# Kernel tuning notes

Measured on AMD Instinct MI355X. Metric: run time of the kernel, lower is better.

Reference implementation:

```python
import jax, jax.numpy as jnp
import numpy as np

LATENT = 512
MEL = 80


def _lstm(x, Wk, Wr, b):
    # x: [B, T, Din]; Keras gate order i, f, g(cell), o
    B = x.shape[0]
    D = Wr.shape[0]
    h0 = jnp.zeros((B, D), x.dtype)
    c0 = jnp.zeros((B, D), x.dtype)

    def step(carry, xt):
        h, c = carry
        z = xt @ Wk + h @ Wr + b  # [B, 4D]
        i, f, g, o = jnp.split(z, 4, axis=-1)
        i = jax.nn.sigmoid(i)
        f = jax.nn.sigmoid(f)
        g = jnp.tanh(g)
        o = jax.nn.sigmoid(o)
        c = f * c + i * g
        h = o * jnp.tanh(c)
        return (h, c), h

    (h_f, c_f), hs = jax.lax.scan(step, (h0, c0), x.transpose(1, 0, 2))
    return hs.transpose(1, 0, 2), h_f, c_f  # [B,T,D], [B,D], [B,D]


def setup_inputs() -> dict:
    key = jax.random.key(0)
    ks = jax.random.split(key, 10)
    B, Td, Te, Din, D = 8, 256, 256, MEL, LATENT
    s = lambda k, shp, fan: jax.random.normal(k, shp, jnp.float32) / np.sqrt(fan)
    return {
        "inputs": jax.random.normal(ks[0], (B, Td, Din), jnp.float32),
        "attended_inputs": jax.random.normal(ks[1], (B, Te, D), jnp.float32),
        "lstm_Wk": s(ks[2], (Din, 4 * D), Din),
        "lstm_Wr": s(ks[3], (D, 4 * D), D),
        "lstm_b": jnp.zeros((4 * D,), jnp.float32),
        "W1": s(ks[4], (D, D), D),
        "b1": jnp.zeros((D,), jnp.float32),
        "W3": s(ks[5], (D, 1), D),
        "b3": jnp.zeros((1,), jnp.float32),
        "Wout": s(ks[6], (2 * D, MEL), 2 * D),
        "bout": jnp.zeros((MEL,), jnp.float32),
    }


def reference(inputs, attended_inputs, lstm_Wk, lstm_Wr, lstm_b, W1, b1, W3, b3, Wout, bout):
    x, state_h, state_c = _lstm(inputs, lstm_Wk, lstm_Wr, lstm_b)  # [B,Td,D]
    # NOTE: original code uses dense1 for BOTH projections (dense2 unused)
    half1 = (attended_inputs @ W1 + b1)[:, None, :, :]   # [B,1,Te,D]
    half2 = (x @ W1 + b1)[:, :, None, :]                 # [B,Td,1,D]
    scores = jnp.squeeze(jnp.tanh(half1 + half2) @ W3 + b3, -1)  # [B,Td,Te]
    attn = jax.nn.softmax(scores, axis=-1)
    weighted = jnp.einsum('bde,bef->bdf', attn, attended_inputs)  # [B,Td,D]
    x = jnp.concatenate([x, weighted], axis=2)           # [B,Td,2D]
    out = x @ Wout + bout                                 # [B,Td,MEL]
    return out, state_h, state_c
```

## Files before the change

### kernel.cpp

```cpp
#include <hip/hip_runtime.h>
#include <cstdint>
#include <cmath>

#define TD 256
#define TE 256
#define NB 8
#define DD 512
#define DIN 80
#define NMEL 80

typedef unsigned long long u64;

__device__ __forceinline__ void gemm_body(const float* __restrict__ A,
    const float* __restrict__ B, const float* __restrict__ bias,
    float* __restrict__ C, int N, int K, int m0, int n0)
{
    __shared__ float As[64][17];
    __shared__ __align__(16) float Bs[16][64];
    const int tid = threadIdx.x;
    const int tx = tid & 15, ty = tid >> 4;
    float acc[4][4] = {};
    for (int k0 = 0; k0 < K; k0 += 16) {
#pragma unroll
        for (int i = 0; i < 4; ++i) {
            int lin = tid + i * 256;
            int k = lin & 15, m = lin >> 4;
            As[m][k] = A[(size_t)(m0 + m) * K + k0 + k];
        }
#pragma unroll
        for (int i = 0; i < 4; ++i) {
            int lin = tid + i * 256;
            int n = lin & 63, k = lin >> 6;
            Bs[k][n] = B[(size_t)(k0 + k) * N + n0 + n];
        }
        __syncthreads();
#pragma unroll
        for (int kk = 0; kk < 16; ++kk) {
            float a0 = As[ty * 4 + 0][kk], a1 = As[ty * 4 + 1][kk];
            float a2 = As[ty * 4 + 2][kk], a3 = As[ty * 4 + 3][kk];
            const float4 b4 = *(const float4*)&Bs[kk][tx * 4];
            acc[0][0] += a0 * b4.x; acc[0][1] += a0 * b4.y; acc[0][2] += a0 * b4.z; acc[0][3] += a0 * b4.w;
            acc[1][0] += a1 * b4.x; acc[1][1] += a1 * b4.y; acc[1][2] += a1 * b4.z; acc[1][3] += a1 * b4.w;
            acc[2][0] += a2 * b4.x; acc[2][1] += a2 * b4.y; acc[2][2] += a2 * b4.z; acc[2][3] += a2 * b4.w;
            acc[3][0] += a3 * b4.x; acc[3][1] += a3 * b4.y; acc[3][2] += a3 * b4.z; acc[3][3] += a3 * b4.w;
        }
        __syncthreads();
    }
    const float4 bv = *(const float4*)&bias[n0 + tx * 4];
#pragma unroll
    for (int i = 0; i < 4; ++i) {
        float4 o;
        o.x = acc[i][0] + bv.x; o.y = acc[i][1] + bv.y;
        o.z = acc[i][2] + bv.z; o.w = acc[i][3] + bv.w;
        *(float4*)&C[(size_t)(m0 + ty * 4 + i) * N + n0 + tx * 4] = o;
    }
}

__global__ __launch_bounds__(256) void gemm_bias_k(const float* __restrict__ A,
    const float* __restrict__ B, const float* __restrict__ bias,
    float* __restrict__ C, int N, int K)
{
    gemm_body(A, B, bias, C, N, K, blockIdx.y * 64, blockIdx.x * 64);
}

__global__ __launch_bounds__(256) void fused_pre_k(
    const float* __restrict__ inputs, const float* __restrict__ Wk,
    const float* __restrict__ lb, float* __restrict__ Zx,
    const float* __restrict__ att, const float* __restrict__ W1,
    const float* __restrict__ b1, float* __restrict__ half1)
{
    int wg = blockIdx.x;
    if (wg < 1024) {
        gemm_body(inputs, Wk, lb, Zx, 2048, 80, (wg >> 5) * 64, (wg & 31) * 64);
    } else {
        wg -= 1024;
        gemm_body(att, W1, b1, half1, 512, 512, (wg >> 3) * 64, (wg & 7) * 64);
    }
}

__global__ __launch_bounds__(256, 1) void lstm_k(const float* __restrict__ Zx,
    const float* __restrict__ Wr, float* __restrict__ hs,
    u64* __restrict__ hpub,
    float* __restrict__ outh, float* __restrict__ outc)
{
    __shared__ __align__(16) float h_s[512];
    __shared__ float part[256];
    const int b = blockIdx.x & 7;
    const int g = blockIdx.x >> 3;
    const int tid = threadIdx.x;
    const int wv = tid >> 6;
    const int lane = tid & 63;
    const int gcol = ((lane >> 4) << 9) | (g << 4) | (lane & 15);
    const int col = (g << 4) | (lane & 15);

    float w[128];
    {
        const float* wb = Wr + (size_t)(wv * 128) * 2048 + gcol;
#pragma unroll
        for (int i = 0; i < 128; ++i) w[i] = wb[(size_t)i * 2048];
    }
    float creg = 0.f, hlast = 0.f;
    u64* const pub0 = hpub + (size_t)b * 512;
    u64* const pub1 = hpub + (size_t)(8 + b) * 512;

    for (int t = 0; t < TD; ++t) {
        float zx = 0.f;
        if (wv == 0) zx = Zx[(size_t)(b * TD + t) * 2048 + gcol];

        {
            u64* const pr = (t & 1) ? pub1 : pub0;
            const unsigned stag = (unsigned)t;
            u64 v0 = 0, v1 = 0;
            bool d0 = false, d1 = false;
            for (;;) {
                if (!d0) { v0 = __hip_atomic_load(pr + tid, __ATOMIC_RELAXED, __HIP_MEMORY_SCOPE_AGENT);
                           d0 = ((unsigned)(v0 >> 32) == stag); }
                if (!d1) { v1 = __hip_atomic_load(pr + tid + 256, __ATOMIC_RELAXED, __HIP_MEMORY_SCOPE_AGENT);
                           d1 = ((unsigned)(v1 >> 32) == stag); }
                if (d0 && d1) break;
                __builtin_amdgcn_s_sleep(1);
            }
            h_s[tid]       = __uint_as_float((unsigned)v0);
            h_s[tid + 256] = __uint_as_float((unsigned)v1);
        }
        __syncthreads();

        float acc = 0.f;
        {
            const float4* h4 = (const float4*)(h_s + (wv << 7));
#pragma unroll
            for (int i = 0; i < 32; ++i) {
                float4 h = h4[i];
                acc += w[4 * i + 0] * h.x;
                acc += w[4 * i + 1] * h.y;
                acc += w[4 * i + 2] * h.z;
                acc += w[4 * i + 3] * h.w;
            }
        }
        part[tid] = acc;
        __syncthreads();
        if (wv == 0) {
            float z = part[lane] + part[64 + lane] + part[128 + lane] + part[192 + lane] + zx;
            float zf = __shfl(z, lane + 16);
            float zg = __shfl(z, lane + 32);
            float zo = __shfl(z, lane + 48);
            if (lane < 16) {
                float ig = 1.f / (1.f + expf(-z));
                float fg = 1.f / (1.f + expf(-zf));
                float gg = tanhf(zg);
                float og = 1.f / (1.f + expf(-zo));
                creg = fg * creg + ig * gg;
                hlast = og * tanhf(creg);
                u64 pv = ((u64)(unsigned)(t + 1) << 32) | (u64)__float_as_uint(hlast);
                u64* const pw = (t & 1) ? pub0 : pub1;
                __hip_atomic_store(pw + col, pv, __ATOMIC_RELAXED, __HIP_MEMORY_SCOPE_AGENT);
                hs[(size_t)(b * TD + t) * 512 + col] = hlast;
            }
        }
    }
    if (wv == 0 && lane < 16) {
        outh[b * 512 + col] = hlast;
        outc[b * 512 + col] = creg;
    }
}

__global__ __launch_bounds__(256) void attn_k(const float* __restrict__ half1,
    const float* __restrict__ half2, const float* __restrict__ att,
    const float* __restrict__ W3, const float* __restrict__ b3,
    float* __restrict__ wgt)
{
    __shared__ __align__(16) float h2s[4][512];
    __shared__ float h1s[256 * 33];
    __shared__ __align__(16) float sc[4][256];
    __shared__ __align__(16) float av[8][512];
    const int tid = threadIdx.x;
    const int bb = blockIdx.x >> 6;
    const int d0 = (blockIdx.x & 63) * 4;
    const float C2 = 2.885390081777927f;

#pragma unroll
    for (int i = 0; i < 8; ++i) {
        int lin = tid + i * 256;
        int r = lin >> 9, k = lin & 511;
        h2s[r][k] = half2[(size_t)(bb * TD + d0 + r) * 512 + k] * C2;
    }

    float accs[4] = {0.f, 0.f, 0.f, 0.f};
    for (int kc = 0; kc < 512; kc += 32) {
#pragma unroll
        for (int i = 0; i < 32; ++i) {
            int lin = tid + i * 256;
            int e = lin >> 5, kk = lin & 31;
            h1s[e * 33 + kk] = half1[(size_t)(bb * TE + e) * 512 + kc + kk] * C2;
        }
        __syncthreads();
        const float* myh1 = h1s + tid * 33;
#pragma unroll 8
        for (int kk = 0; kk < 32; ++kk) {
            float u = myh1[kk];
            float w = W3[kc + kk];
#pragma unroll
            for (int r = 0; r < 4; ++r) {
                float t = 1.f - 2.f * __builtin_amdgcn_rcpf(__builtin_amdgcn_exp2f(u + h2s[r][kc + kk]) + 1.f);
                accs[r] += t * w;
            }
        }
        __syncthreads();
    }
    {
        const float b3v = b3[0];
#pragma unroll
        for (int r = 0; r < 4; ++r) sc[r][tid] = accs[r] + b3v;
    }
    __syncthreads();
    {
        const int r = tid >> 6, l = tid & 63;
        float4 v = *(const float4*)&sc[r][l * 4];
        float mx = fmaxf(fmaxf(v.x, v.y), fmaxf(v.z, v.w));
#pragma unroll
        for (int off = 32; off; off >>= 1) mx = fmaxf(mx, __shfl_xor(mx, off));
        const float L2E = 1.44269504089f;
        float e0 = __builtin_amdgcn_exp2f((v.x - mx) * L2E);
        float e1 = __builtin_amdgcn_exp2f((v.y - mx) * L2E);
        float e2 = __builtin_amdgcn_exp2f((v.z - mx) * L2E);
        float e3 = __builtin_amdgcn_exp2f((v.w - mx) * L2E);
        float s = e0 + e1 + e2 + e3;
#pragma unroll
        for (int off = 32; off; off >>= 1) s += __shfl_xor(s, off);
        float inv = 1.f / s;
        float4 p; p.x = e0 * inv; p.y = e1 * inv; p.z = e2 * inv; p.w = e3 * inv;
        *(float4*)&sc[r][l * 4] = p;
    }
    __syncthreads();
    float acc[4][2] = {};
    for (int e0 = 0; e0 < TE; e0 += 8) {
#pragma unroll
        for (int i = 0; i < 16; ++i) {
            int lin = tid + i * 256;
            int e = lin >> 9, k = lin & 511;
            av[e][k] = att[(size_t)(bb * TE + e0 + e) * 512 + k];
        }
        __syncthreads();
#pragma unroll
        for (int ee = 0; ee < 8; ++ee) {
            float x0 = av[ee][tid], x1 = av[ee][tid + 256];
#pragma unroll
            for (int r = 0; r < 4; ++r) {
                float p = sc[r][e0 + ee];
                acc[r][0] += p * x0;
                acc[r][1] += p * x1;
            }
        }
        __syncthreads();
    }
#pragma unroll
    for (int r = 0; r < 4; ++r) {
        wgt[(size_t)(bb * TD + d0 + r) * 512 + tid] = acc[r][0];
        wgt[(size_t)(bb * TD + d0 + r) * 512 + tid + 256] = acc[r][1];
    }
}

__global__ __launch_bounds__(256) void outgemm_k(const float* __restrict__ x,
    const float* __restrict__ wgt, const float* __restrict__ Wout,
    const float* __restrict__ bout, float* __restrict__ out)
{
    __shared__ float As[64][17];
    __shared__ float Bs[16][80];
    const int tid = threadIdx.x;
    const int tx = tid & 15, ty = tid >> 4;
    const int m0 = blockIdx.x * 64;
    const int ks = blockIdx.y;
    float acc[4][5] = {};
    for (int kt = 0; kt < 16; ++kt) {
        const int k0 = ks * 256 + kt * 16;
        const float* src = (k0 < 512) ? x : wgt;
        const int kk0 = (k0 < 512) ? k0 : (k0 - 512);
#pragma unroll
        for (int i = 0; i < 4; ++i) {
            int lin = tid + i * 256;
            int k = lin & 15, m = lin >> 4;
            As[m][k] = src[(size_t)(m0 + m) * 512 + kk0 + k];
        }
#pragma unroll
        for (int i = 0; i < 5; ++i) {
            int lin = tid + i * 256;
            int n = lin % 80, k = lin / 80;
            Bs[k][n] = Wout[(size_t)(k0 + k) * 80 + n];
        }
        __syncthreads();
#pragma unroll
        for (int kk = 0; kk < 16; ++kk) {
            float a[4], bv[5];
#pragma unroll
            for (int i = 0; i < 4; ++i) a[i] = As[ty * 4 + i][kk];
#pragma unroll
            for (int j = 0; j < 5; ++j) bv[j] = Bs[kk][tx * 5 + j];
#pragma unroll
            for (int i = 0; i < 4; ++i)
#pragma unroll
                for (int j = 0; j < 5; ++j) acc[i][j] += a[i] * bv[j];
        }
        __syncthreads();
    }
#pragma unroll
    for (int i = 0; i < 4; ++i) {
#pragma unroll
        for (int j = 0; j < 5; ++j) {
            float v = acc[i][j];
            if (ks == 0) v += bout[tx * 5 + j];
            atomicAdd(&out[(size_t)(m0 + ty * 4 + i) * 80 + tx * 5 + j], v);
        }
    }
}

extern "C" void kernel_launch(void* const* d_in, const int* in_sizes, int n_in,
                              void* d_out, int out_size, void* d_ws, size_t ws_size,
                              hipStream_t stream)
{
    (void)in_sizes; (void)n_in; (void)out_size; (void)ws_size;
    const float* inputs = (const float*)d_in[0];
    const float* att    = (const float*)d_in[1];
    const float* Wk     = (const float*)d_in[2];
    const float* Wr     = (const float*)d_in[3];
    const float* lb     = (const float*)d_in[4];
    const float* W1     = (const float*)d_in[5];
    const float* b1     = (const float*)d_in[6];
    const float* W3     = (const float*)d_in[7];
    const float* b3     = (const float*)d_in[8];
    const float* Wout   = (const float*)d_in[9];
    const float* bout   = (const float*)d_in[10];

    float* out  = (float*)d_out;
    float* outh = out + 2048 * 80;
    float* outc = outh + 8 * 512;

    char* ws = (char*)d_ws;
    float* Zx    = (float*)(ws);
    float* half1 = (float*)(ws + (16u << 20));
    float* half2 = (float*)(ws + (20u << 20));
    float* hsx   = (float*)(ws + (24u << 20));
    float* wgt   = (float*)(ws + (28u << 20));
    u64*   hpub  = (u64*)(ws + (32u << 20));

    (void)hipMemsetAsync(ws + (32u << 20), 0, 2 * 8 * 512 * sizeof(u64), stream);
    (void)hipMemsetAsync(d_out, 0, (size_t)2048 * 80 * 4, stream);

    fused_pre_k<<<dim3(1280), 256, 0, stream>>>(inputs, Wk, lb, Zx, att, W1, b1, half1);

    void* args[] = { (void*)&Zx, (void*)&Wr, (void*)&hsx, (void*)&hpub,
                     (void*)&outh, (void*)&outc };
    (void)hipLaunchCooperativeKernel((void*)lstm_k, dim3(256), dim3(256), args, 0, stream);

    gemm_bias_k<<<dim3(8, 32), 256, 0, stream>>>(hsx, W1, b1, half2, 512, 512);
    attn_k<<<dim3(512), 256, 0, stream>>>(half1, half2, att, W3, b3, wgt);
    outgemm_k<<<dim3(32, 4), 256, 0, stream>>>(hsx, wgt, Wout, bout, out);
}
```

Measured before the change: 912.1 us.

## Fuse all stages into one cooperative persistent kernel with grid syncs

Merges the pre-GEMM, LSTM recurrence, half2 GEMM, attention and output GEMM into a single cooperative kernel of 256 workgroups. Stages are separated by grid.sync, and shared memory is carved from one pool. This removes four kernel launches and the gaps between them. In exchange, every stage now runs at 256 workgroups with launch_bounds(256,1) and a large shared pool, which can hurt the GEMM and attention phases that previously used more blocks and higher occupancy. The old multi-kernel path is kept as a fallback if the cooperative launch fails.

```diff
diff --git a/kernel.cpp b/kernel.cpp
--- a/kernel.cpp
+++ b/kernel.cpp
@@ -1,6 +1,9 @@
 #include <hip/hip_runtime.h>
+#include <hip/hip_cooperative_groups.h>
 #include <cstdint>
 #include <cmath>
+
+namespace cg = cooperative_groups;
 
 #define TD 256
 #define TE 256
@@ -11,12 +14,14 @@
 
 typedef unsigned long long u64;
 
+#define SMEM_POOL_BYTES 46080
+
 __device__ __forceinline__ void gemm_body(const float* __restrict__ A,
     const float* __restrict__ B, const float* __restrict__ bias,
-    float* __restrict__ C, int N, int K, int m0, int n0)
-{
-    __shared__ float As[64][17];
-    __shared__ __align__(16) float Bs[16][64];
+    float* __restrict__ C, int N, int K, int m0, int n0, char* sm)
+{
+    float (*As)[17] = (float(*)[17])sm;
+    float (*Bs)[64] = (float(*)[64])(sm + 4352);
     const int tid = threadIdx.x;
     const int tx = tid & 15, ty = tid >> 4;
     float acc[4][4] = {};
@@ -56,37 +61,15 @@
     }
 }
 
-__global__ __launch_bounds__(256) void gemm_bias_k(const float* __restrict__ A,
-    const float* __restrict__ B, const float* __restrict__ bias,
-    float* __restrict__ C, int N, int K)
-{
-    gemm_body(A, B, bias, C, N, K, blockIdx.y * 64, blockIdx.x * 64);
-}
-
-__global__ __launch_bounds__(256) void fused_pre_k(
-    const float* __restrict__ inputs, const float* __restrict__ Wk,
-    const float* __restrict__ lb, float* __restrict__ Zx,
-    const float* __restrict__ att, const float* __restrict__ W1,
-    const float* __restrict__ b1, float* __restrict__ half1)
-{
-    int wg = blockIdx.x;
-    if (wg < 1024) {
-        gemm_body(inputs, Wk, lb, Zx, 2048, 80, (wg >> 5) * 64, (wg & 31) * 64);
-    } else {
-        wg -= 1024;
-        gemm_body(att, W1, b1, half1, 512, 512, (wg >> 3) * 64, (wg & 7) * 64);
-    }
-}
-
-__global__ __launch_bounds__(256, 1) void lstm_k(const float* __restrict__ Zx,
+__device__ __forceinline__ void lstm_body(const float* __restrict__ Zx,
     const float* __restrict__ Wr, float* __restrict__ hs,
-    u64* __restrict__ hpub,
-    float* __restrict__ outh, float* __restrict__ outc)
-{
-    __shared__ __align__(16) float h_s[512];
-    __shared__ float part[256];
-    const int b = blockIdx.x & 7;
-    const int g = blockIdx.x >> 3;
+    u64* __restrict__ hpub, float* __restrict__ outh, float* __restrict__ outc,
+    int wg, char* sm)
+{
+    float* h_s  = (float*)sm;
+    float* part = (float*)(sm + 2048);
+    const int b = wg & 7;
+    const int g = wg >> 3;
     const int tid = threadIdx.x;
     const int wv = tid >> 6;
     const int lane = tid & 63;
@@ -164,18 +147,16 @@
     }
 }
 
-__global__ __launch_bounds__(256) void attn_k(const float* __restrict__ half1,
+__device__ __forceinline__ void attn_body(const float* __restrict__ half1,
     const float* __restrict__ half2, const float* __restrict__ att,
     const float* __restrict__ W3, const float* __restrict__ b3,
-    float* __restrict__ wgt)
-{
-    __shared__ __align__(16) float h2s[4][512];
-    __shared__ float h1s[256 * 33];
-    __shared__ __align__(16) float sc[4][256];
-    __shared__ __align__(16) float av[8][512];
+    float* __restrict__ wgt, int bb, int d0, char* sm)
+{
+    float (*h2s)[512] = (float(*)[512])sm;
+    float (*sc)[256]  = (float(*)[256])(sm + 8192);
+    float *h1s        = (float*)(sm + 12288);
+    float (*av)[512]  = (float(*)[512])(sm + 12288);
     const int tid = threadIdx.x;
-    const int bb = blockIdx.x >> 6;
-    const int d0 = (blockIdx.x & 63) * 4;
     const float C2 = 2.885390081777927f;
 
 #pragma unroll
@@ -260,16 +241,15 @@
     }
 }
 
-__global__ __launch_bounds__(256) void outgemm_k(const float* __restrict__ x,
+__device__ __forceinline__ void outgemm_body(const float* __restrict__ x,
     const float* __restrict__ wgt, const float* __restrict__ Wout,
-    const float* __restrict__ bout, float* __restrict__ out)
-{
-    __shared__ float As[64][17];
-    __shared__ float Bs[16][80];
+    const float* __restrict__ bout, float* __restrict__ out, int m0, int ks,
+    char* sm)
+{
+    float (*As2)[17] = (float(*)[17])sm;
+    float (*Bs2)[80] = (float(*)[80])(sm + 4352);
     const int tid = threadIdx.x;
     const int tx = tid & 15, ty = tid >> 4;
-    const int m0 = blockIdx.x * 64;
-    const int ks = blockIdx.y;
     float acc[4][5] = {};
     for (int kt = 0; kt < 16; ++kt) {
         const int k0 = ks * 256 + kt * 16;
@@ -279,22 +259,22 @@
         for (int i = 0; i < 4; ++i) {
             int lin = tid + i * 256;
             int k = lin & 15, m = lin >> 4;
-            As[m][k] = src[(size_t)(m0 + m) * 512 + kk0 + k];
+            As2[m][k] = src[(size_t)(m0 + m) * 512 + kk0 + k];
         }
 #pragma unroll
         for (int i = 0; i < 5; ++i) {
             int lin = tid + i * 256;
             int n = lin % 80, k = lin / 80;
-            Bs[k][n] = Wout[(size_t)(k0 + k) * 80 + n];
+            Bs2[k][n] = Wout[(size_t)(k0 + k) * 80 + n];
         }
         __syncthreads();
 #pragma unroll
         for (int kk = 0; kk < 16; ++kk) {
             float a[4], bv[5];
 #pragma unroll
-            for (int i = 0; i < 4; ++i) a[i] = As[ty * 4 + i][kk];
-#pragma unroll
-            for (int j = 0; j < 5; ++j) bv[j] = Bs[kk][tx * 5 + j];
+            for (int i = 0; i < 4; ++i) a[i] = As2[ty * 4 + i][kk];
+#pragma unroll
+            for (int j = 0; j < 5; ++j) bv[j] = Bs2[kk][tx * 5 + j];
 #pragma unroll
             for (int i = 0; i < 4; ++i)
 #pragma unroll
@@ -311,6 +291,96 @@
             atomicAdd(&out[(size_t)(m0 + ty * 4 + i) * 80 + tx * 5 + j], v);
         }
     }
+}
+
+__global__ __launch_bounds__(256, 1) void mega_k(
+    const float* __restrict__ inputs, const float* __restrict__ Wk,
+    const float* __restrict__ lb, const float* __restrict__ att,
+    const float* __restrict__ W1, const float* __restrict__ b1,
+    const float* __restrict__ Wr, const float* __restrict__ W3,
+    const float* __restrict__ b3, const float* __restrict__ Wout,
+    const float* __restrict__ bout,
+    float* __restrict__ Zx, float* __restrict__ half1,
+    float* __restrict__ half2, float* __restrict__ hsx,
+    float* __restrict__ wgt, u64* __restrict__ hpub,
+    float* __restrict__ out, float* __restrict__ outh, float* __restrict__ outc)
+{
+    __shared__ __align__(16) char smem[SMEM_POOL_BYTES];
+    const int wg = blockIdx.x;
+    cg::grid_group grid = cg::this_grid();
+
+    for (int job = wg; job < 1280; job += 256) {
+        if (job < 1024)
+            gemm_body(inputs, Wk, lb, Zx, 2048, 80, (job >> 5) * 64, (job & 31) * 64, smem);
+        else {
+            int j = job - 1024;
+            gemm_body(att, W1, b1, half1, 512, 512, (j >> 3) * 64, (j & 7) * 64, smem);
+        }
+    }
+    grid.sync();
+
+    lstm_body(Zx, Wr, hsx, hpub, outh, outc, wg, smem);
+    grid.sync();
+
+    gemm_body(hsx, W1, b1, half2, 512, 512, (wg >> 3) * 64, (wg & 7) * 64, smem);
+    grid.sync();
+
+    for (int job = wg; job < 512; job += 256)
+        attn_body(half1, half2, att, W3, b3, wgt, job >> 6, (job & 63) * 4, smem);
+    grid.sync();
+
+    if (wg < 128)
+        outgemm_body(hsx, wgt, Wout, bout, out, (wg >> 2) * 64, wg & 3, smem);
+}
+
+__global__ __launch_bounds__(256) void gemm_bias_k(const float* __restrict__ A,
+    const float* __restrict__ B, const float* __restrict__ bias,
+    float* __restrict__ C, int N, int K)
+{
+    __shared__ __align__(16) char pool[8448];
+    gemm_body(A, B, bias, C, N, K, blockIdx.y * 64, blockIdx.x * 64, pool);
+}
+
+__global__ __launch_bounds__(256) void fused_pre_k(
+    const float* __restrict__ inputs, const float* __restrict__ Wk,
+    const float* __restrict__ lb, float* __restrict__ Zx,
+    const float* __restrict__ att, const float* __restrict__ W1,
+    const float* __restrict__ b1, float* __restrict__ half1)
+{
+    __shared__ __align__(16) char pool[8448];
+    int wg = blockIdx.x;
+    if (wg < 1024)
+        gemm_body(inputs, Wk, lb, Zx, 2048, 80, (wg >> 5) * 64, (wg & 31) * 64, pool);
+    else {
+        wg -= 1024;
+        gemm_body(att, W1, b1, half1, 512, 512, (wg >> 3) * 64, (wg & 7) * 64, pool);
+    }
+}
+
+__global__ __launch_bounds__(256, 1) void lstm_k(const float* __restrict__ Zx,
+    const float* __restrict__ Wr, float* __restrict__ hs,
+    u64* __restrict__ hpub, float* __restrict__ outh, float* __restrict__ outc)
+{
+    __shared__ __align__(16) char pool[3072];
+    lstm_body(Zx, Wr, hs, hpub, outh, outc, blockIdx.x, pool);
+}
+
+__global__ __launch_bounds__(256) void attn_k(const float* __restrict__ half1,
+    const float* __restrict__ half2, const float* __restrict__ att,
+    const float* __restrict__ W3, const float* __restrict__ b3,
+    float* __restrict__ wgt)
+{
+    __shared__ __align__(16) char pool[SMEM_POOL_BYTES];
+    attn_body(half1, half2, att, W3, b3, wgt, blockIdx.x >> 6,
+              (blockIdx.x & 63) * 4, pool);
+}
+
+__global__ __launch_bounds__(256) void outgemm_k(const float* __restrict__ x,
+    const float* __restrict__ wgt, const float* __restrict__ Wout,
+    const float* __restrict__ bout, float* __restrict__ out)
+{
+    __shared__ __align__(16) char pool[9472];
+    outgemm_body(x, wgt, Wout, bout, out, blockIdx.x * 64, blockIdx.y, pool);
 }
 
 extern "C" void kernel_launch(void* const* d_in, const int* in_sizes, int n_in,
@@ -342,16 +412,24 @@
     float* wgt   = (float*)(ws + (28u << 20));
     u64*   hpub  = (u64*)(ws + (32u << 20));
 
-    (void)hipMemsetAsync(ws + (32u << 20), 0, 2 * 8 * 512 * sizeof(u64), stream);
+    (void)hipMemsetAsync(ws + (32u << 20), 0, 65536, stream);
     (void)hipMemsetAsync(d_out, 0, (size_t)2048 * 80 * 4, stream);
 
-    fused_pre_k<<<dim3(1280), 256, 0, stream>>>(inputs, Wk, lb, Zx, att, W1, b1, half1);
-
-    void* args[] = { (void*)&Zx, (void*)&Wr, (void*)&hsx, (void*)&hpub,
-                     (void*)&outh, (void*)&outc };
-    (void)hipLaunchCooperativeKernel((void*)lstm_k, dim3(256), dim3(256), args, 0, stream);
-
-    gemm_bias_k<<<dim3(8, 32), 256, 0, stream>>>(hsx, W1, b1, half2, 512, 512);
-    attn_k<<<dim3(512), 256, 0, stream>>>(half1, half2, att, W3, b3, wgt);
-    outgemm_k<<<dim3(32, 4), 256, 0, stream>>>(hsx, wgt, Wout, bout, out);
-}
+    void* args[] = {
+        (void*)&inputs, (void*)&Wk, (void*)&lb, (void*)&att, (void*)&W1,
+        (void*)&b1, (void*)&Wr, (void*)&W3, (void*)&b3, (void*)&Wout,
+        (void*)&bout, (void*)&Zx, (void*)&half1, (void*)&half2, (void*)&hsx,
+        (void*)&wgt, (void*)&hpub, (void*)&out, (void*)&outh, (void*)&outc
+    };
+    hipError_t cerr = hipLaunchCooperativeKernel((void*)mega_k, dim3(256),
+                                                 dim3(256), args, 0, stream);
+    if (cerr != hipSuccess) {
+        fused_pre_k<<<dim3(1280), 256, 0, stream>>>(inputs, Wk, lb, Zx, att, W1, b1, half1);
+        void* largs[] = { (void*)&Zx, (void*)&Wr, (void*)&hsx, (void*)&hpub,
+                          (void*)&outh, (void*)&outc };
+        (void)hipLaunchCooperativeKernel((void*)lstm_k, dim3(256), dim3(256), largs, 0, stream);
+        gemm_bias_k<<<dim3(8, 32), 256, 0, stream>>>(hsx, W1, b1, half2, 512, 512);
+        attn_k<<<dim3(512), 256, 0, stream>>>(half1, half2, att, W3, b3, wgt);
+        outgemm_k<<<dim3(32, 4), 256, 0, stream>>>(hsx, wgt, Wout, bout, out);
+    }
+}
```

Result: slower. 1.090 ms (+19.5%).
